# Kernel tuning notes

Hardware: AMD Instinct MI355X
Metric: run time of the kernel (lower is better)

The kernel has to match this reference:

```python
import jax, jax.numpy as jnp
import numpy as np

N, D, E = 100000, 64, 1250000  # nodes, feature dim, total signed edges
H = D // 2                     # per-polarity hidden dim


def _mean_agg(x, src, dst, n):
    """Mean-aggregate messages x[src] at dst over n segments (gather->scatter)."""
    s = jax.ops.segment_sum(x[src], dst, num_segments=n)
    cnt = jax.ops.segment_sum(jnp.ones((src.shape[0], 1), x.dtype), dst, num_segments=n)
    return s / jnp.maximum(cnt, 1.0)


def _lin_w(k, fi, fo):
    b = 1.0 / np.sqrt(fi)
    return jax.random.uniform(k, (fi, fo), jnp.float32, -b, b)


def setup_inputs() -> dict:
    key = jax.random.key(0)
    ks = list(jax.random.split(key, 24))
    init_emb = jax.random.normal(ks[0], (N, D), dtype=jnp.float32)
    src = jax.random.randint(ks[1], (E,), 0, N)
    dst = jax.random.randint(ks[2], (E,), 0, N)
    sign = jnp.where(jax.random.uniform(ks[3], (E,)) < 0.5, 1, -1)
    edge_index_s = jnp.stack([src, dst, sign], axis=1)
    return dict(
        init_emb=init_emb,
        edge_index_s=edge_index_s,
        # conv1 (first_aggr=True): lin([mean_agg, x]) per polarity -> H
        Wp1=_lin_w(ks[4], 2 * D, H), bp1=jnp.zeros((H,), jnp.float32),
        Wn1=_lin_w(ks[5], 2 * D, H), bn1=jnp.zeros((H,), jnp.float32),
        # rest conv: lin([agg_pos, agg_neg, x_half]) per polarity -> H
        Wp2=_lin_w(ks[6], 3 * H, H), bp2=jnp.zeros((H,), jnp.float32),
        Wn2=_lin_w(ks[7], 3 * H, H), bn2=jnp.zeros((H,), jnp.float32),
        # final linear D->D
        Ww=_lin_w(ks[8], D, D), bw=jnp.zeros((D,), jnp.float32),
        # MLP readout: Linear+BN+ReLU, Linear+BN+ReLU, Linear->1 (inference mode)
        Wm1=_lin_w(ks[9], D, D), bm1=jnp.zeros((D,), jnp.float32),
        g1=jnp.ones((D,), jnp.float32), be1=jnp.zeros((D,), jnp.float32),
        rm1=jnp.zeros((D,), jnp.float32), rv1=jnp.ones((D,), jnp.float32),
        Wm2=_lin_w(ks[10], D, D), bm2=jnp.zeros((D,), jnp.float32),
        g2=jnp.ones((D,), jnp.float32), be2=jnp.zeros((D,), jnp.float32),
        rm2=jnp.zeros((D,), jnp.float32), rv2=jnp.ones((D,), jnp.float32),
        Wm3=_lin_w(ks[11], D, 1), bm3=jnp.zeros((1,), jnp.float32),
    )


def reference(init_emb, edge_index_s, Wp1, bp1, Wn1, bn1, Wp2, bp2, Wn2, bn2,
              Ww, bw, Wm1, bm1, g1, be1, rm1, rv1, Wm2, bm2, g2, be2, rm2, rv2,
              Wm3, bm3):
    # split signed edge list into pos / neg edge indices (eager boolean mask,
    # mirrors edge_index_s[edge_index_s[:,2]>0][:, :2].t())
    sign = edge_index_s[:, 2]
    pos = edge_index_s[sign > 0]
    neg = edge_index_s[sign < 0]
    ps, pd = pos[:, 0], pos[:, 1]
    ns, nd = neg[:, 0], neg[:, 1]

    x = init_emb
    # --- first signed conv (first_aggr=True) ---
    ap = _mean_agg(x, ps, pd, N)
    an = _mean_agg(x, ns, nd, N)
    hp = jnp.concatenate([ap, x], -1) @ Wp1 + bp1
    hn = jnp.concatenate([an, x], -1) @ Wn1 + bn1
    z = jnp.tanh(jnp.concatenate([hp, hn], -1))  # [N, D]

    # --- rest signed conv (balance-theory cross-polarity aggregation) ---
    xp, xn = z[:, :H], z[:, H:]
    hp = jnp.concatenate([_mean_agg(xp, ps, pd, N), _mean_agg(xn, ns, nd, N), xp], -1) @ Wp2 + bp2
    hn = jnp.concatenate([_mean_agg(xn, ps, pd, N), _mean_agg(xp, ns, nd, N), xn], -1) @ Wn2 + bn2
    z = jnp.tanh(jnp.concatenate([hp, hn], -1))  # [N, D]

    # --- final linear + tanh ---
    z = jnp.tanh(z @ Ww + bw)

    # --- MLP readout (inference: BN uses running stats, dropout disabled) ---
    def bn(h, g, b, rm, rv):
        return (h - rm) * jax.lax.rsqrt(rv + 1e-5) * g + b

    h = jax.nn.relu(bn(z @ Wm1 + bm1, g1, be1, rm1, rv1))
    h = jax.nn.relu(bn(h @ Wm2 + bm2, g2, be2, rm2, rv2))
    prob = jax.nn.sigmoid(h @ Wm3 + bm3)  # [N, 1]
    return z, prob
```

## Files before the change

kernel.cpp:

```cpp
#include <hip/hip_runtime.h>
#include <hip/hip_bf16.h>

#define CAP 32

typedef __attribute__((ext_vector_type(8))) short bf16x8;
typedef __attribute__((ext_vector_type(4))) float f32x4;

#define MFMA(a, b, c) __builtin_amdgcn_mfma_f32_16x16x32_bf16(a, b, c, 0, 0, 0)

__device__ __forceinline__ unsigned short bf16rn(float f) {
    unsigned u = __builtin_bit_cast(unsigned, f);
    u += 0x7fffu + ((u >> 16) & 1u);
    return (unsigned short)(u >> 16);
}

__device__ __forceinline__ bf16x8 packbf8(const float* p) {
    bf16x8 r;
    #pragma unroll
    for (int j = 0; j < 8; ++j) r[j] = (short)bf16rn(p[j]);
    return r;
}

__device__ __forceinline__ bf16x8 wfrag(const float* __restrict__ W, int NN,
                                        int kt, int ct, int q, int c) {
    const float* base = W + (kt * 32 + q * 8) * NN + ct * 16 + c;
    float t[8];
    #pragma unroll
    for (int j = 0; j < 8; ++j) t[j] = base[j * NN];
    return packbf8(t);
}

__device__ __forceinline__ bf16x8 afrag_bf16(const __hip_bfloat16* row, int cw, int q) {
    return *(const bf16x8*)((const short*)row + cw + q * 8);
}
__device__ __forceinline__ bf16x8 afrag_f32(const float* row, int cw, int q) {
    float t[8];
    *(float4*)(t)     = *(const float4*)(row + cw + q * 8);
    *(float4*)(t + 4) = *(const float4*)(row + cw + q * 8 + 4);
    return packbf8(t);
}

__global__ __launch_bounds__(256) void pg_build(
    const int* __restrict__ ei,
    int* __restrict__ plist, int* __restrict__ nlist,
    int* __restrict__ pcur, int* __restrict__ ncur, int E)
{
    int e = blockIdx.x * 256 + threadIdx.x;
    if (e >= E) return;
    int s  = ei[3 * e + 0];
    int d  = ei[3 * e + 1];
    int sg = ei[3 * e + 2];
    if (sg > 0) {
        int slot = atomicAdd(pcur + d, 1);
        if (slot < CAP) plist[d * CAP + slot] = s;
    } else {
        int slot = atomicAdd(ncur + d, 1);
        if (slot < CAP) nlist[d * CAP + slot] = s;
    }
}

__global__ __launch_bounds__(256, 6) void pg_gather(
    const float* __restrict__ src,
    const int* __restrict__ plist, const int* __restrict__ nlist,
    const int* __restrict__ pcur, const int* __restrict__ ncur,
    __hip_bfloat16* __restrict__ agg, int N)
{
    int tid = threadIdx.x;
    int w = tid >> 6, lane = tid & 63;

    #pragma unroll 1
    for (int g = 0; g < 4; ++g) {
        int i0 = blockIdx.x * 64 + w * 16 + g * 4;
        int pd[4], nd[4], pde[4], nde[4], pl[4], nl[4];
        #pragma unroll
        for (int n = 0; n < 4; ++n) {
            int i = min(i0 + n, N - 1);
            pd[n] = __builtin_amdgcn_readfirstlane(pcur[i]);
            nd[n] = __builtin_amdgcn_readfirstlane(ncur[i]);
            pde[n] = min(pd[n], CAP);
            nde[n] = min(nd[n], CAP);
            const int* plrow = plist + (size_t)i * CAP;
            const int* nlrow = nlist + (size_t)i * CAP;
            pl[n] = plrow[lane & 31];
            nl[n] = nlrow[lane & 31];
        }
        int maxd = 0;
        #pragma unroll
        for (int n = 0; n < 4; ++n) maxd = max(maxd, max(pde[n], nde[n]));

        float ps[4] = {0.f, 0.f, 0.f, 0.f}, ns[4] = {0.f, 0.f, 0.f, 0.f};
        #pragma unroll 1
        for (int e = 0; e < maxd; e += 4) {
            float pv[4][4], nv[4][4];
            #pragma unroll
            for (int n = 0; n < 4; ++n) {
                #pragma unroll
                for (int k = 0; k < 4; ++k) {
                    int idx = e + k;
                    int psl = (idx < pde[n]) ? idx : 0;
                    int nsl = (idx < nde[n]) ? idx : 0;
                    unsigned sp = (unsigned)__builtin_amdgcn_readlane(pl[n], psl);
                    unsigned sn = (unsigned)__builtin_amdgcn_readlane(nl[n], nsl);
                    sp = sp < (unsigned)N ? sp : 0u;
                    sn = sn < (unsigned)N ? sn : 0u;
                    const float* prow = src + ((size_t)sp << 6);
                    const float* nrow = src + ((size_t)sn << 6);
                    pv[n][k] = prow[lane];
                    nv[n][k] = nrow[lane];
                }
            }
            #pragma unroll
            for (int n = 0; n < 4; ++n) {
                #pragma unroll
                for (int k = 0; k < 4; ++k) {
                    int idx = e + k;
                    float wp  = (idx < pde[n]) ? 1.f : 0.f;
                    float wn_ = (idx < nde[n]) ? 1.f : 0.f;
                    ps[n] = fmaf(wp,  pv[n][k], ps[n]);
                    ns[n] = fmaf(wn_, nv[n][k], ns[n]);
                }
            }
        }
        #pragma unroll
        for (int n = 0; n < 4; ++n) {
            int i = i0 + n;
            if (i < N) {
                __hip_bfloat16* arow = agg + ((size_t)i << 7);
                arow[lane]      = __float2bfloat16(ps[n] / fmaxf((float)pd[n], 1.f));
                arow[64 + lane] = __float2bfloat16(ns[n] / fmaxf((float)nd[n], 1.f));
            }
        }
    }
}

__global__ __launch_bounds__(256, 3) void pg_gemm1(
    const float* __restrict__ x, const __hip_bfloat16* __restrict__ agg,
    const float* __restrict__ Wp, const float* __restrict__ bp,
    const float* __restrict__ Wn, const float* __restrict__ bn,
    float* __restrict__ z1, int N, int nwv)
{
    int tid = threadIdx.x;
    int w = tid >> 6, lane = tid & 63;
    int q = lane >> 4, c = lane & 15;

    bf16x8 B[2][4][2];
    #pragma unroll
    for (int kt = 0; kt < 4; ++kt)
        #pragma unroll
        for (int ct = 0; ct < 2; ++ct) {
            B[0][kt][ct] = wfrag(Wp, 32, kt, ct, q, c);
            B[1][kt][ct] = wfrag(Wn, 32, kt, ct, q, c);
        }
    float bias[2][2];
    #pragma unroll
    for (int ct = 0; ct < 2; ++ct) {
        bias[0][ct] = bp[ct * 16 + c];
        bias[1][ct] = bn[ct * 16 + c];
    }

    int ntiles = (N + 15) >> 4;
    #pragma unroll 1
    for (int t = blockIdx.x * 4 + w; t < ntiles; t += nwv) {
        int i = min(t * 16 + c, N - 1);
        const __hip_bfloat16* arow = agg + ((size_t)i << 7);
        const float* xrow = x + ((size_t)i << 6);
        bf16x8 aA0 = afrag_bf16(arow, 0, q);
        bf16x8 aA1 = afrag_bf16(arow, 32, q);
        bf16x8 aA2 = afrag_bf16(arow, 64, q);
        bf16x8 aA3 = afrag_bf16(arow, 96, q);
        bf16x8 aX0 = afrag_f32(xrow, 0, q);
        bf16x8 aX1 = afrag_f32(xrow, 32, q);
        f32x4 acc[2][2];
        #pragma unroll
        for (int ct = 0; ct < 2; ++ct) {
            f32x4 a = {0.f, 0.f, 0.f, 0.f};
            a = MFMA(aA0, B[0][0][ct], a);
            a = MFMA(aA1, B[0][1][ct], a);
            a = MFMA(aX0, B[0][2][ct], a);
            a = MFMA(aX1, B[0][3][ct], a);
            acc[0][ct] = a;
            f32x4 b = {0.f, 0.f, 0.f, 0.f};
            b = MFMA(aA2, B[1][0][ct], b);
            b = MFMA(aA3, B[1][1][ct], b);
            b = MFMA(aX0, B[1][2][ct], b);
            b = MFMA(aX1, B[1][3][ct], b);
            acc[1][ct] = b;
        }
        #pragma unroll
        for (int h = 0; h < 2; ++h)
            #pragma unroll
            for (int ct = 0; ct < 2; ++ct)
                #pragma unroll
                for (int r = 0; r < 4; ++r) {
                    int row = t * 16 + q * 4 + r;
                    if (row < N)
                        z1[(size_t)row * 64 + h * 32 + ct * 16 + c] =
                            tanhf(acc[h][ct][r] + bias[h][ct]);
                }
    }
}

__global__ __launch_bounds__(256, 3) void pg_gemm2(
    float* zio, const __hip_bfloat16* __restrict__ agg,
    const float* __restrict__ Wp2, const float* __restrict__ bp2,
    const float* __restrict__ Wn2, const float* __restrict__ bn2,
    int N, int nwv)
{
    int tid = threadIdx.x;
    int w = tid >> 6, lane = tid & 63;
    int q = lane >> 4, c = lane & 15;

    bf16x8 B[2][3][2];
    #pragma unroll
    for (int kt = 0; kt < 3; ++kt)
        #pragma unroll
        for (int ct = 0; ct < 2; ++ct) {
            B[0][kt][ct] = wfrag(Wp2, 32, kt, ct, q, c);
            B[1][kt][ct] = wfrag(Wn2, 32, kt, ct, q, c);
        }
    float bias[2][2];
    #pragma unroll
    for (int ct = 0; ct < 2; ++ct) {
        bias[0][ct] = bp2[ct * 16 + c];
        bias[1][ct] = bn2[ct * 16 + c];
    }

    int ntiles = (N + 15) >> 4;
    #pragma unroll 1
    for (int t = blockIdx.x * 4 + w; t < ntiles; t += nwv) {
        int i = min(t * 16 + c, N - 1);
        const __hip_bfloat16* arow = agg + ((size_t)i << 7);
        const float* zrow = zio + ((size_t)i << 6);
        bf16x8 ap0 = afrag_bf16(arow, 0, q);
        bf16x8 ap1 = afrag_bf16(arow, 96, q);
        bf16x8 an0 = afrag_bf16(arow, 32, q);
        bf16x8 an1 = afrag_bf16(arow, 64, q);
        bf16x8 az0 = afrag_f32(zrow, 0, q);
        bf16x8 az1 = afrag_f32(zrow, 32, q);
        f32x4 acc[2][2];
        #pragma unroll
        for (int ct = 0; ct < 2; ++ct) {
            f32x4 a = {0.f, 0.f, 0.f, 0.f};
            a = MFMA(ap0, B[0][0][ct], a);
            a = MFMA(ap1, B[0][1][ct], a);
            a = MFMA(az0, B[0][2][ct], a);
            acc[0][ct] = a;
            f32x4 b = {0.f, 0.f, 0.f, 0.f};
            b = MFMA(an0, B[1][0][ct], b);
            b = MFMA(an1, B[1][1][ct], b);
            b = MFMA(az1, B[1][2][ct], b);
            acc[1][ct] = b;
        }
        #pragma unroll
        for (int h = 0; h < 2; ++h)
            #pragma unroll
            for (int ct = 0; ct < 2; ++ct)
                #pragma unroll
                for (int r = 0; r < 4; ++r) {
                    int row = t * 16 + q * 4 + r;
                    if (row < N)
                        zio[(size_t)row * 64 + h * 32 + ct * 16 + c] =
                            tanhf(acc[h][ct][r] + bias[h][ct]);
                }
    }
}

__global__ __launch_bounds__(256, 2) void pg_mlp(
    float* out,
    const float* __restrict__ Ww,  const float* __restrict__ bw,
    const float* __restrict__ Wm1, const float* __restrict__ bm1,
    const float* __restrict__ g1,  const float* __restrict__ be1,
    const float* __restrict__ rm1, const float* __restrict__ rv1,
    const float* __restrict__ Wm2, const float* __restrict__ bm2,
    const float* __restrict__ g2,  const float* __restrict__ be2,
    const float* __restrict__ rm2, const float* __restrict__ rv2,
    const float* __restrict__ Wm3, const float* __restrict__ bm3,
    int N, int nwv)
{
    __shared__ float xpos[4][16][68];
    int tid = threadIdx.x;
    int w = tid >> 6, lane = tid & 63;
    int q = lane >> 4, c = lane & 15;
    float (*lx)[68] = xpos[w];

    bf16x8 Bw[2][4], B1[2][4], B2[2][4];
    #pragma unroll
    for (int kt = 0; kt < 2; ++kt)
        #pragma unroll
        for (int ct = 0; ct < 4; ++ct) {
            Bw[kt][ct] = wfrag(Ww,  64, kt, ct, q, c);
            B1[kt][ct] = wfrag(Wm1, 64, kt, ct, q, c);
            B2[kt][ct] = wfrag(Wm2, 64, kt, ct, q, c);
        }
    float bwv[4], s1[4], o1[4], s2[4], o2[4], w3[4];
    #pragma unroll
    for (int ct = 0; ct < 4; ++ct) {
        int cc = ct * 16 + c;
        bwv[ct] = bw[cc];
        float a = g1[cc] * rsqrtf(rv1[cc] + 1e-5f);
        s1[ct] = a; o1[ct] = (bm1[cc] - rm1[cc]) * a + be1[cc];
        float b = g2[cc] * rsqrtf(rv2[cc] + 1e-5f);
        s2[ct] = b; o2[ct] = (bm2[cc] - rm2[cc]) * b + be2[cc];
        w3[ct] = Wm3[cc];
    }
    float b3 = bm3[0];

    int ntiles = (N + 15) >> 4;
    #pragma unroll 1
    for (int t = blockIdx.x * 4 + w; t < ntiles; t += nwv) {
        int i = min(t * 16 + c, N - 1);
        const float* zrow = out + ((size_t)i << 6);
        bf16x8 a0 = afrag_f32(zrow, 0, q);
        bf16x8 a1 = afrag_f32(zrow, 32, q);
        f32x4 acc[4];

        #pragma unroll
        for (int ct = 0; ct < 4; ++ct) {
            f32x4 a = {0.f, 0.f, 0.f, 0.f};
            a = MFMA(a0, Bw[0][ct], a);
            a = MFMA(a1, Bw[1][ct], a);
            acc[ct] = a;
        }
        #pragma unroll
        for (int ct = 0; ct < 4; ++ct)
            #pragma unroll
            for (int r = 0; r < 4; ++r) {
                int row = t * 16 + q * 4 + r;
                float v = tanhf(acc[ct][r] + bwv[ct]);
                if (row < N) out[(size_t)row * 64 + ct * 16 + c] = v;
                lx[q * 4 + r][ct * 16 + c] = v;
            }
        {
            const float* pr = &lx[c][0];
            float tb[8];
            *(float4*)tb       = *(const float4*)(pr + q * 8);
            *(float4*)(tb + 4) = *(const float4*)(pr + q * 8 + 4);
            a0 = packbf8(tb);
            *(float4*)tb       = *(const float4*)(pr + 32 + q * 8);
            *(float4*)(tb + 4) = *(const float4*)(pr + 32 + q * 8 + 4);
            a1 = packbf8(tb);
        }

        #pragma unroll
        for (int ct = 0; ct < 4; ++ct) {
            f32x4 a = {0.f, 0.f, 0.f, 0.f};
            a = MFMA(a0, B1[0][ct], a);
            a = MFMA(a1, B1[1][ct], a);
            acc[ct] = a;
        }
        #pragma unroll
        for (int ct = 0; ct < 4; ++ct)
            #pragma unroll
            for (int r = 0; r < 4; ++r)
                lx[q * 4 + r][ct * 16 + c] = fmaxf(acc[ct][r] * s1[ct] + o1[ct], 0.f);
        {
            const float* pr = &lx[c][0];
            float tb[8];
            *(float4*)tb       = *(const float4*)(pr + q * 8);
            *(float4*)(tb + 4) = *(const float4*)(pr + q * 8 + 4);
            a0 = packbf8(tb);
            *(float4*)tb       = *(const float4*)(pr + 32 + q * 8);
            *(float4*)(tb + 4) = *(const float4*)(pr + 32 + q * 8 + 4);
            a1 = packbf8(tb);
        }

        #pragma unroll
        for (int ct = 0; ct < 4; ++ct) {
            f32x4 a = {0.f, 0.f, 0.f, 0.f};
            a = MFMA(a0, B2[0][ct], a);
            a = MFMA(a1, B2[1][ct], a);
            acc[ct] = a;
        }
        float tr[4];
        #pragma unroll
        for (int r = 0; r < 4; ++r) {
            float hs = 0.f;
            #pragma unroll
            for (int ct = 0; ct < 4; ++ct) {
                float h2 = fmaxf(acc[ct][r] * s2[ct] + o2[ct], 0.f);
                hs = fmaf(h2, w3[ct], hs);
            }
            tr[r] = hs;
        }
        #pragma unroll
        for (int m = 1; m < 16; m <<= 1)
            #pragma unroll
            for (int r = 0; r < 4; ++r) tr[r] += __shfl_xor(tr[r], m, 16);
        if (c == 0) {
            #pragma unroll
            for (int r = 0; r < 4; ++r) {
                int row = t * 16 + q * 4 + r;
                if (row < N)
                    out[(size_t)N * 64 + row] = 1.f / (1.f + expf(-(tr[r] + b3)));
            }
        }
    }
}

extern "C" void kernel_launch(void* const* d_in, const int* in_sizes, int n_in,
                              void* d_out, int out_size, void* d_ws, size_t ws_size,
                              hipStream_t stream) {
    const float* x   = (const float*)d_in[0];
    const int*   ei  = (const int*)  d_in[1];
    const float* Wp1 = (const float*)d_in[2];
    const float* bp1 = (const float*)d_in[3];
    const float* Wn1 = (const float*)d_in[4];
    const float* bn1 = (const float*)d_in[5];
    const float* Wp2 = (const float*)d_in[6];
    const float* bp2 = (const float*)d_in[7];
    const float* Wn2 = (const float*)d_in[8];
    const float* bn2 = (const float*)d_in[9];
    const float* Ww  = (const float*)d_in[10];
    const float* bw  = (const float*)d_in[11];
    const float* Wm1 = (const float*)d_in[12];
    const float* bm1 = (const float*)d_in[13];
    const float* g1  = (const float*)d_in[14];
    const float* be1 = (const float*)d_in[15];
    const float* rm1 = (const float*)d_in[16];
    const float* rv1 = (const float*)d_in[17];
    const float* Wm2 = (const float*)d_in[18];
    const float* bm2 = (const float*)d_in[19];
    const float* g2  = (const float*)d_in[20];
    const float* be2 = (const float*)d_in[21];
    const float* rm2 = (const float*)d_in[22];
    const float* rv2 = (const float*)d_in[23];
    const float* Wm3 = (const float*)d_in[24];
    const float* bm3 = (const float*)d_in[25];
    float* out = (float*)d_out;

    int N = in_sizes[0] / 64;
    int E = in_sizes[1] / 3;

    int* plist = (int*)d_ws;
    int* nlist = plist + (size_t)N * CAP;
    int* pcur  = nlist + (size_t)N * CAP;
    int* ncur  = pcur + N;
    __hip_bfloat16* agg = (__hip_bfloat16*)(ncur + N);
    float* zio = out;

    hipMemsetAsync(pcur, 0, 2 * (size_t)N * sizeof(int), stream);

    pg_build<<<(E + 255) / 256, 256, 0, stream>>>(ei, plist, nlist, pcur, ncur, E);

    int nb = (N + 63) / 64;
    const int gb = 512, nwv = gb * 4;
    pg_gather<<<nb, 256, 0, stream>>>(x, plist, nlist, pcur, ncur, agg, N);
    pg_gemm1<<<gb, 256, 0, stream>>>(x, agg, Wp1, bp1, Wn1, bn1, zio, N, nwv);
    pg_gather<<<nb, 256, 0, stream>>>(zio, plist, nlist, pcur, ncur, agg, N);
    pg_gemm2<<<gb, 256, 0, stream>>>(zio, agg, Wp2, bp2, Wn2, bn2, N, nwv);
    pg_mlp<<<gb, 256, 0, stream>>>(out, Ww, bw,
                                   Wm1, bm1, g1, be1, rm1, rv1,
                                   Wm2, bm2, g2, be2, rm2, rv2,
                                   Wm3, bm3, N, nwv);
}
```

Before: 274.4 us.

## Store node features and intermediate activations in bf16 to halve gather traffic

Adds a cast kernel that converts the input embeddings to bf16, and switches the gather and GEMM stages to read bf16 rows. The first and second conv outputs are now written as bf16, with z1 in the output buffer and z2 packed into the aggregation buffer, replacing fp32 intermediates. The goal is to halve the bytes moved by the random-row gathers and the activation reads. The cost is an extra cast pass, extra rounding of activations before aggregation, and reuse of the output buffer as scratch space, which could be fragile if pg_mlp writes out while other rows are still being read.

Result: faster. 257.4 us (-6.2%).

```diff
diff --git a/kernel.cpp b/kernel.cpp
--- a/kernel.cpp
+++ b/kernel.cpp
@@ -33,11 +33,18 @@
 __device__ __forceinline__ bf16x8 afrag_bf16(const __hip_bfloat16* row, int cw, int q) {
     return *(const bf16x8*)((const short*)row + cw + q * 8);
 }
-__device__ __forceinline__ bf16x8 afrag_f32(const float* row, int cw, int q) {
-    float t[8];
-    *(float4*)(t)     = *(const float4*)(row + cw + q * 8);
-    *(float4*)(t + 4) = *(const float4*)(row + cw + q * 8 + 4);
-    return packbf8(t);
+
+__global__ __launch_bounds__(256) void pg_cast(
+    const float* __restrict__ x, __hip_bfloat16* __restrict__ xb, int n)
+{
+    int i = (blockIdx.x * 256 + threadIdx.x) * 4;
+    if (i < n) {
+        float4 v = *(const float4*)(x + i);
+        ushort4 o;
+        o.x = bf16rn(v.x); o.y = bf16rn(v.y);
+        o.z = bf16rn(v.z); o.w = bf16rn(v.w);
+        *(ushort4*)((unsigned short*)xb + i) = o;
+    }
 }
 
 __global__ __launch_bounds__(256) void pg_build(
@@ -50,17 +57,14 @@
     int s  = ei[3 * e + 0];
     int d  = ei[3 * e + 1];
     int sg = ei[3 * e + 2];
-    if (sg > 0) {
-        int slot = atomicAdd(pcur + d, 1);
-        if (slot < CAP) plist[d * CAP + slot] = s;
-    } else {
-        int slot = atomicAdd(ncur + d, 1);
-        if (slot < CAP) nlist[d * CAP + slot] = s;
-    }
+    int* cur  = (sg > 0) ? pcur : ncur;
+    int* list = (sg > 0) ? plist : nlist;
+    int slot = atomicAdd(cur + d, 1);
+    if (slot < CAP) list[(size_t)d * CAP + slot] = s;
 }
 
 __global__ __launch_bounds__(256, 6) void pg_gather(
-    const float* __restrict__ src,
+    const __hip_bfloat16* __restrict__ src,
     const int* __restrict__ plist, const int* __restrict__ nlist,
     const int* __restrict__ pcur, const int* __restrict__ ncur,
     __hip_bfloat16* __restrict__ agg, int N)
@@ -103,10 +107,10 @@
                     unsigned sn = (unsigned)__builtin_amdgcn_readlane(nl[n], nsl);
                     sp = sp < (unsigned)N ? sp : 0u;
                     sn = sn < (unsigned)N ? sn : 0u;
-                    const float* prow = src + ((size_t)sp << 6);
-                    const float* nrow = src + ((size_t)sn << 6);
-                    pv[n][k] = prow[lane];
-                    nv[n][k] = nrow[lane];
+                    const __hip_bfloat16* prow = src + ((size_t)sp << 6);
+                    const __hip_bfloat16* nrow = src + ((size_t)sn << 6);
+                    pv[n][k] = __bfloat162float(prow[lane]);
+                    nv[n][k] = __bfloat162float(nrow[lane]);
                 }
             }
             #pragma unroll
@@ -134,10 +138,10 @@
 }
 
 __global__ __launch_bounds__(256, 3) void pg_gemm1(
-    const float* __restrict__ x, const __hip_bfloat16* __restrict__ agg,
+    const __hip_bfloat16* __restrict__ xb, const __hip_bfloat16* __restrict__ agg,
     const float* __restrict__ Wp, const float* __restrict__ bp,
     const float* __restrict__ Wn, const float* __restrict__ bn,
-    float* __restrict__ z1, int N, int nwv)
+    __hip_bfloat16* __restrict__ z1b, int N, int nwv)
 {
     int tid = threadIdx.x;
     int w = tid >> 6, lane = tid & 63;
@@ -163,13 +167,13 @@
     for (int t = blockIdx.x * 4 + w; t < ntiles; t += nwv) {
         int i = min(t * 16 + c, N - 1);
         const __hip_bfloat16* arow = agg + ((size_t)i << 7);
-        const float* xrow = x + ((size_t)i << 6);
+        const __hip_bfloat16* xrow = xb + ((size_t)i << 6);
         bf16x8 aA0 = afrag_bf16(arow, 0, q);
         bf16x8 aA1 = afrag_bf16(arow, 32, q);
         bf16x8 aA2 = afrag_bf16(arow, 64, q);
         bf16x8 aA3 = afrag_bf16(arow, 96, q);
-        bf16x8 aX0 = afrag_f32(xrow, 0, q);
-        bf16x8 aX1 = afrag_f32(xrow, 32, q);
+        bf16x8 aX0 = afrag_bf16(xrow, 0, q);
+        bf16x8 aX1 = afrag_bf16(xrow, 32, q);
         f32x4 acc[2][2];
         #pragma unroll
         for (int ct = 0; ct < 2; ++ct) {
@@ -194,14 +198,14 @@
                 for (int r = 0; r < 4; ++r) {
                     int row = t * 16 + q * 4 + r;
                     if (row < N)
-                        z1[(size_t)row * 64 + h * 32 + ct * 16 + c] =
-                            tanhf(acc[h][ct][r] + bias[h][ct]);
+                        z1b[(size_t)row * 64 + h * 32 + ct * 16 + c] =
+                            __float2bfloat16(tanhf(acc[h][ct][r] + bias[h][ct]));
                 }
     }
 }
 
 __global__ __launch_bounds__(256, 3) void pg_gemm2(
-    float* zio, const __hip_bfloat16* __restrict__ agg,
+    const __hip_bfloat16* __restrict__ z1b, __hip_bfloat16* agg,
     const float* __restrict__ Wp2, const float* __restrict__ bp2,
     const float* __restrict__ Wn2, const float* __restrict__ bn2,
     int N, int nwv)
@@ -230,13 +234,13 @@
     for (int t = blockIdx.x * 4 + w; t < ntiles; t += nwv) {
         int i = min(t * 16 + c, N - 1);
         const __hip_bfloat16* arow = agg + ((size_t)i << 7);
-        const float* zrow = zio + ((size_t)i << 6);
+        const __hip_bfloat16* zrow = z1b + ((size_t)i << 6);
         bf16x8 ap0 = afrag_bf16(arow, 0, q);
         bf16x8 ap1 = afrag_bf16(arow, 96, q);
         bf16x8 an0 = afrag_bf16(arow, 32, q);
         bf16x8 an1 = afrag_bf16(arow, 64, q);
-        bf16x8 az0 = afrag_f32(zrow, 0, q);
-        bf16x8 az1 = afrag_f32(zrow, 32, q);
+        bf16x8 az0 = afrag_bf16(zrow, 0, q);
+        bf16x8 az1 = afrag_bf16(zrow, 32, q);
         f32x4 acc[2][2];
         #pragma unroll
         for (int ct = 0; ct < 2; ++ct) {
@@ -259,14 +263,14 @@
                 for (int r = 0; r < 4; ++r) {
                     int row = t * 16 + q * 4 + r;
                     if (row < N)
-                        zio[(size_t)row * 64 + h * 32 + ct * 16 + c] =
-                            tanhf(acc[h][ct][r] + bias[h][ct]);
+                        agg[(size_t)row * 128 + h * 32 + ct * 16 + c] =
+                            __float2bfloat16(tanhf(acc[h][ct][r] + bias[h][ct]));
                 }
     }
 }
 
 __global__ __launch_bounds__(256, 2) void pg_mlp(
-    float* out,
+    float* out, const __hip_bfloat16* __restrict__ z2b,
     const float* __restrict__ Ww,  const float* __restrict__ bw,
     const float* __restrict__ Wm1, const float* __restrict__ bm1,
     const float* __restrict__ g1,  const float* __restrict__ be1,
@@ -309,9 +313,9 @@
     #pragma unroll 1
     for (int t = blockIdx.x * 4 + w; t < ntiles; t += nwv) {
         int i = min(t * 16 + c, N - 1);
-        const float* zrow = out + ((size_t)i << 6);
-        bf16x8 a0 = afrag_f32(zrow, 0, q);
-        bf16x8 a1 = afrag_f32(zrow, 32, q);
+        const __hip_bfloat16* zrow = z2b + ((size_t)i << 7);
+        bf16x8 a0 = afrag_bf16(zrow, 0, q);
+        bf16x8 a1 = afrag_bf16(zrow, 32, q);
         f32x4 acc[4];
 
         #pragma unroll
@@ -436,19 +440,22 @@
     int* pcur  = nlist + (size_t)N * CAP;
     int* ncur  = pcur + N;
     __hip_bfloat16* agg = (__hip_bfloat16*)(ncur + N);
-    float* zio = out;
+
+    __hip_bfloat16* z1b = (__hip_bfloat16*)out;
+    __hip_bfloat16* xb  = (__hip_bfloat16*)((char*)d_out + (size_t)N * 128);
+
+    pg_cast<<<(N * 64 / 4 + 255) / 256, 256, 0, stream>>>(x, xb, N * 64);
 
     hipMemsetAsync(pcur, 0, 2 * (size_t)N * sizeof(int), stream);
-
     pg_build<<<(E + 255) / 256, 256, 0, stream>>>(ei, plist, nlist, pcur, ncur, E);
 
     int nb = (N + 63) / 64;
     const int gb = 512, nwv = gb * 4;
-    pg_gather<<<nb, 256, 0, stream>>>(x, plist, nlist, pcur, ncur, agg, N);
-    pg_gemm1<<<gb, 256, 0, stream>>>(x, agg, Wp1, bp1, Wn1, bn1, zio, N, nwv);
-    pg_gather<<<nb, 256, 0, stream>>>(zio, plist, nlist, pcur, ncur, agg, N);
-    pg_gemm2<<<gb, 256, 0, stream>>>(zio, agg, Wp2, bp2, Wn2, bn2, N, nwv);
-    pg_mlp<<<gb, 256, 0, stream>>>(out, Ww, bw,
+    pg_gather<<<nb, 256, 0, stream>>>(xb, plist, nlist, pcur, ncur, agg, N);
+    pg_gemm1<<<gb, 256, 0, stream>>>(xb, agg, Wp1, bp1, Wn1, bn1, z1b, N, nwv);
+    pg_gather<<<nb, 256, 0, stream>>>(z1b, plist, nlist, pcur, ncur, agg, N);
+    pg_gemm2<<<gb, 256, 0, stream>>>(z1b, agg, Wp2, bp2, Wn2, bn2, N, nwv);
+    pg_mlp<<<gb, 256, 0, stream>>>(out, agg, Ww, bw,
                                    Wm1, bm1, g1, be1, rm1, rv1,
                                    Wm2, bm2, g2, be2, rm2, rv2,
                                    Wm3, bm3, N, nwv);
```
